# Optimization experiments

Hardware: AMD Instinct MI355X
Metric: run time of the kernel (lower is better)

Reference implementation:

```python
import jax, jax.numpy as jnp
import numpy as np

B, S, D, H = 2, 2048, 1024, 16
HD = D // H  # head dim = 64


def setup_inputs() -> dict:
    key = jax.random.key(0)
    ks = jax.random.split(key, 9)
    std = 0.02
    return {
        "hidden_states": jax.random.normal(ks[0], (B, S, D), jnp.float32),
        "wq": jax.random.normal(ks[1], (D, D), jnp.float32) * std,
        "bq": jnp.zeros((D,), jnp.float32),
        "wk": jax.random.normal(ks[2], (D, D), jnp.float32) * std,
        "bk": jnp.zeros((D,), jnp.float32),
        "wv": jax.random.normal(ks[3], (D, D), jnp.float32) * std,
        "bv": jnp.zeros((D,), jnp.float32),
        "wo": jax.random.normal(ks[4], (D, D), jnp.float32) * std,
        "bo": jnp.zeros((D,), jnp.float32),
    }


def reference(hidden_states, wq, bq, wk, bk, wv, bv, wo, bo):
    b, s, d = hidden_states.shape
    # projections (torch Linear: x @ W.T + b; here weights stored as [in,out]-equivalent transpose)
    q = hidden_states @ wq.T + bq
    k = hidden_states @ wk.T + bk
    v = hidden_states @ wv.T + bv
    # [b, h, s, hd]
    q = q.reshape(b, s, H, HD).transpose(0, 2, 1, 3)
    k = k.reshape(b, s, H, HD).transpose(0, 2, 1, 3)
    v = v.reshape(b, s, H, HD).transpose(0, 2, 1, 3)
    scores = jnp.einsum("bhqd,bhkd->bhqk", q, k) / jnp.sqrt(jnp.float32(HD))
    probs = jax.nn.softmax(scores, axis=-1)  # dropout p=0 (eval)
    ctx = jnp.einsum("bhqk,bhkd->bhqd", probs, v)
    ctx = ctx.transpose(0, 2, 1, 3).reshape(b, s, d)
    return ctx @ wo.T + bo
```

## Files before the change

### kernel.cpp

```cpp
#include <hip/hip_runtime.h>
#include <math.h>
#include <stdint.h>

constexpr int BB  = 2;
constexpr int SS  = 2048;
constexpr int DD  = 1024;
constexpr int HH  = 16;
constexpr int HDD = 64;
constexpr int MM  = BB * SS;

typedef uint16_t u16;
typedef __attribute__((ext_vector_type(4))) float    f32x4;
typedef __attribute__((ext_vector_type(8))) _Float16 f16x8;
typedef __attribute__((ext_vector_type(4))) _Float16 f16x4;
typedef __attribute__((ext_vector_type(8))) short    s16x8;
typedef __attribute__((ext_vector_type(4))) unsigned int u32x4;

__device__ __forceinline__ u16 to_f16(float f) {
    const _Float16 h = (_Float16)f;
    return __builtin_bit_cast(u16, h);
}

__device__ __forceinline__ f32x4 mfma32(s16x8 a, s16x8 b, f32x4 c) {
    return __builtin_amdgcn_mfma_f32_16x16x32_f16(
        __builtin_bit_cast(f16x8, a), __builtin_bit_cast(f16x8, b), c, 0, 0, 0);
}
__device__ __forceinline__ f32x4 mfma32_ff(s16x8 a, f16x8 b, f32x4 c) {
    return __builtin_amdgcn_mfma_f32_16x16x32_f16(
        __builtin_bit_cast(f16x8, a), b, c, 0, 0, 0);
}

__device__ __forceinline__ void load_lds16(const void* g, void* l) {
    __builtin_amdgcn_global_load_lds(
        (const __attribute__((address_space(1))) void*)g,
        (__attribute__((address_space(3))) void*)l, 16, 0, 0);
}

__global__ __launch_bounds__(256) void cast_all(
    const float* __restrict__ x,
    const float* __restrict__ w0, const float* __restrict__ w1,
    const float* __restrict__ w2, const float* __restrict__ w3,
    u16* __restrict__ xb, u16* __restrict__ wb)
{
    const int blk = blockIdx.x, tid = threadIdx.x;
    const float* src; u16* dst; int idx;
    if (blk < 2048) { src = x; dst = xb; idx = blk * 256 + tid; }
    else {
        const int b2 = blk - 2048, which = b2 >> 9;
        src = (which == 0) ? w0 : (which == 1) ? w1 : (which == 2) ? w2 : w3;
        dst = wb + ((size_t)which << 20);
        idx = (b2 & 511) * 256 + tid;
    }
    const float4* in4 = (const float4*)src;
    const float4 a = in4[idx * 2], b = in4[idx * 2 + 1];
    s16x8 v;
    v[0] = (short)to_f16(a.x); v[1] = (short)to_f16(a.y);
    v[2] = (short)to_f16(a.z); v[3] = (short)to_f16(a.w);
    v[4] = (short)to_f16(b.x); v[5] = (short)to_f16(b.y);
    v[6] = (short)to_f16(b.z); v[7] = (short)to_f16(b.w);
    *(s16x8*)(dst + (size_t)idx * 8) = v;
}

template <bool SWAP>
__device__ __forceinline__ void kloop(
    const u16* __restrict__ Ag, const u16* __restrict__ Wg,
    u16* Abase, u16* Bbase, const int K, const int KH,
    const int c0, const int c1,
    const int lane, const int wm, const int wn, f32x4 (&acc)[4][4])
{
    load_lds16(Ag + (size_t)c0 * 16 * K, Abase + c0 * 512);
    load_lds16(Ag + (size_t)c1 * 16 * K, Abase + c1 * 512);
    load_lds16(Wg + (size_t)c0 * 16 * K, Bbase + c0 * 512);
    load_lds16(Wg + (size_t)c1 * 16 * K, Bbase + c1 * 512);

    for (int k0 = 0; k0 < KH; k0 += 32) {
        const int buf = (k0 >> 5) & 1;
        __syncthreads();
        if (k0 + 32 < KH) {
            const int nb_ = (buf ^ 1) * 4096;
            load_lds16(Ag + (size_t)c0 * 16 * K + k0 + 32, Abase + nb_ + c0 * 512);
            load_lds16(Ag + (size_t)c1 * 16 * K + k0 + 32, Abase + nb_ + c1 * 512);
            load_lds16(Wg + (size_t)c0 * 16 * K + k0 + 32, Bbase + nb_ + c0 * 512);
            load_lds16(Wg + (size_t)c1 * 16 * K + k0 + 32, Bbase + nb_ + c1 * 512);
        }
        const u16* Acur = Abase + buf * 4096;
        const u16* Bcur = Bbase + buf * 4096;

        s16x8 af[4], bf4[4];
#pragma unroll
        for (int i = 0; i < 4; ++i) {
            const int row = wm + i * 16 + (lane & 15);
            const int u   = (lane >> 4) ^ (row & 3);
            af[i] = *(const s16x8*)(Acur + (size_t)row * 32 + u * 8);
        }
#pragma unroll
        for (int j = 0; j < 4; ++j) {
            const int row = wn + j * 16 + (lane & 15);
            const int u   = (lane >> 4) ^ (row & 3);
            bf4[j] = *(const s16x8*)(Bcur + (size_t)row * 32 + u * 8);
        }
#pragma unroll
        for (int i = 0; i < 4; ++i)
#pragma unroll
            for (int j = 0; j < 4; ++j)
                acc[i][j] = SWAP ? mfma32(bf4[j], af[i], acc[i][j])
                                 : mfma32(af[i], bf4[j], acc[i][j]);
    }
}

template <int MODE>
__global__ __launch_bounds__(512) void gemm_mfma(
    const u16* __restrict__ A, const u16* __restrict__ Wb,
    const float* __restrict__ b0, const float* __restrict__ b1,
    const float* __restrict__ b2,
    float* __restrict__ outf, u16* __restrict__ outq, u16* __restrict__ outv,
    const int K)
{
    __shared__ u16 smem[32768];
    u16* As = smem;
    u16* Bs = smem + 16384;

    const int tid = threadIdx.x, lane = tid & 63, wid = tid >> 6;
    const int grp = wid >> 2, w4 = wid & 3;
    const int quad = lane >> 4;
    const int bm = blockIdx.y * 128;
    const int nb = blockIdx.x * 128;
    const int which = nb >> 10;
    const int ncol  = nb & 1023;
    const int KH = K >> 1;
    const u16* Wblk = Wb + ((size_t)which << 20) + (size_t)ncol * K;

    const int srow = lane >> 2;
    const int lu   = (lane & 3) ^ (srow & 3);
    const u16* Ag = A    + (size_t)(bm + srow) * K + grp * KH + lu * 8;
    const u16* Wg = Wblk + (size_t)srow       * K + grp * KH + lu * 8;
    const int c0 = w4 * 2, c1 = c0 + 1;
    u16* Abase = As + grp * 8192;
    u16* Bbase = Bs + grp * 8192;

    f32x4 acc[4][4];
#pragma unroll
    for (int i = 0; i < 4; ++i)
#pragma unroll
        for (int j = 0; j < 4; ++j) { f32x4 z = {0.f, 0.f, 0.f, 0.f}; acc[i][j] = z; }

    const int wm = (w4 >> 1) * 64, wn = (w4 & 1) * 64;
    const bool swap = (MODE == 0) || (which < 2);
    if (swap) kloop<true>(Ag, Wg, Abase, Bbase, K, KH, c0, c1, lane, wm, wn, acc);
    else      kloop<false>(Ag, Wg, Abase, Bbase, K, KH, c0, c1, lane, wm, wn, acc);

    __syncthreads();
    float* rp = (float*)smem;
    const int slot = (w4 * 64 + lane) * 4;
    if (grp == 1) {
#pragma unroll
        for (int i = 0; i < 4; ++i)
#pragma unroll
            for (int j = 0; j < 4; ++j)
                *(f32x4*)(rp + (i * 4 + j) * 1024 + slot) = acc[i][j];
    }
    __syncthreads();
    if (grp != 0) return;
#pragma unroll
    for (int i = 0; i < 4; ++i)
#pragma unroll
        for (int j = 0; j < 4; ++j)
            acc[i][j] += *(const f32x4*)(rp + (i * 4 + j) * 1024 + slot);

    if (MODE == 0) {
#pragma unroll
        for (int j = 0; j < 4; ++j) {
            const int n0 = nb + wn + 16 * j + quad * 4;
            const float4 bv = *(const float4*)&b0[n0];
#pragma unroll
            for (int i = 0; i < 4; ++i) {
                const int m = bm + wm + 16 * i + (lane & 15);
                f32x4 w = acc[i][j];
                w[0] += bv.x; w[1] += bv.y; w[2] += bv.z; w[3] += bv.w;
                *(f32x4*)&outf[(size_t)m * 1024 + n0] = w;
            }
        }
    } else if (which < 2) {
        const float* bias = which ? b1 : b0;
        const float scale = which ? 1.0f : 0.125f;
        u16* outb = outq + ((size_t)which << 22);
        const int h = (ncol + wn) >> 6;
#pragma unroll
        for (int j = 0; j < 4; ++j) {
            const int nl0 = ncol + wn + 16 * j + quad * 4;
            const float4 bv = *(const float4*)&bias[nl0];
            const int hd0 = 16 * j + quad * 4;
#pragma unroll
            for (int i = 0; i < 4; ++i) {
                const int m = bm + wm + 16 * i + (lane & 15);
                const int b_ = m >> 11, s = m & 2047;
                f16x4 w;
                w[0] = (_Float16)((acc[i][j][0] + bv.x) * scale);
                w[1] = (_Float16)((acc[i][j][1] + bv.y) * scale);
                w[2] = (_Float16)((acc[i][j][2] + bv.z) * scale);
                w[3] = (_Float16)((acc[i][j][3] + bv.w) * scale);
                *(f16x4*)&outb[(((size_t)(b_ * HH + h)) * SS + s) * HDD + hd0] = w;
            }
        }
    } else {
        const int kt = ((bm + wm) & 2047) >> 6;
        const int b_ = (bm + wm) >> 11;
#pragma unroll
        for (int j = 0; j < 4; ++j) {
            const int nl = ncol + wn + 16 * j + (lane & 15);
            const float bb = b2[nl];
            const int h = nl >> 6, hd = nl & 63;
            u16* vrow = outv + (((size_t)(b_ * HH + h)) * HDD + hd) * SS + kt * 64;
#pragma unroll
            for (int i = 0; i < 4; ++i) {
                const int p0 = (i >> 1) * 32 + quad * 8 + (i & 1) * 4;
                f16x4 w;
                w[0] = (_Float16)(acc[i][j][0] + bb);
                w[1] = (_Float16)(acc[i][j][1] + bb);
                w[2] = (_Float16)(acc[i][j][2] + bb);
                w[3] = (_Float16)(acc[i][j][3] + bb);
                *(f16x4*)&vrow[p0] = w;
            }
        }
    }
}

__global__ __launch_bounds__(512, 4) void attn_mfma(
    const u16* __restrict__ Q, const u16* __restrict__ Kg,
    const u16* __restrict__ Vt, u16* __restrict__ ctx)
{
    __shared__ u16 smem[32768];

    const int tid = threadIdx.x, lane = tid & 63, wid = tid >> 6;
    const int grp = wid >> 2, w4 = wid & 3;
    const int quad = lane >> 4;
    const int bh = blockIdx.y, q0 = blockIdx.x * 128;
    const u16* Qb = Q  + (size_t)bh * SS * HDD;
    const u16* Kb = Kg + (size_t)bh * SS * HDD + (size_t)grp * 1024 * HDD;
    const u16* Vb = Vt + (size_t)bh * HDD * SS + grp * 1024;

    u16* Kbase = smem + grp * 8192;
    u16* Vbase = smem + 16384 + grp * 8192;

    const int qa = q0 + w4 * 32 + (lane & 15);
    const s16x8 bq0a = *(const s16x8*)(Qb + (size_t)qa * HDD + quad * 8);
    const s16x8 bq1a = *(const s16x8*)(Qb + (size_t)qa * HDD + 32 + quad * 8);
    const s16x8 bq0b = *(const s16x8*)(Qb + (size_t)(qa + 16) * HDD + quad * 8);
    const s16x8 bq1b = *(const s16x8*)(Qb + (size_t)(qa + 16) * HDD + 32 + quad * 8);

    f32x4 oa[4], ob[4];
    f32x4 la4 = {0.f, 0.f, 0.f, 0.f}, lb4 = {0.f, 0.f, 0.f, 0.f};
#pragma unroll
    for (int m = 0; m < 4; ++m) {
        f32x4 z = {0.f, 0.f, 0.f, 0.f};
        oa[m] = z; ob[m] = z;
    }
    const s16x8 ones = {15360, 15360, 15360, 15360,
                        15360, 15360, 15360, 15360};

    const int c0 = w4 * 2, c1 = c0 + 1;
    const int r0 = (c0 * 64 + lane) >> 3, lu0 = ((lane & 7) ^ (r0 & 7));
    const int r1 = (c1 * 64 + lane) >> 3, lu1 = ((lane & 7) ^ (r1 & 7));
    const u16* Kp0 = Kb + (size_t)r0 * HDD + lu0 * 8;
    const u16* Kp1 = Kb + (size_t)r1 * HDD + lu1 * 8;
    const u16* Vp0 = Vb + (size_t)r0 * SS + lu0 * 8;
    const u16* Vp1 = Vb + (size_t)r1 * SS + lu1 * 8;

    load_lds16(Kp0, Kbase + c0 * 512);
    load_lds16(Kp1, Kbase + c1 * 512);
    load_lds16(Vp0, Vbase + c0 * 512);
    load_lds16(Vp1, Vbase + c1 * 512);

    for (int kt = 0; kt < 16; ++kt) {
        const int buf = kt & 1;
        __syncthreads();

        if (kt + 1 < 16) {
            const int nb_ = (buf ^ 1) * 4096;
            load_lds16(Kp0 + (size_t)(kt + 1) * 64 * HDD, Kbase + nb_ + c0 * 512);
            load_lds16(Kp1 + (size_t)(kt + 1) * 64 * HDD, Kbase + nb_ + c1 * 512);
            load_lds16(Vp0 + (kt + 1) * 64, Vbase + nb_ + c0 * 512);
            load_lds16(Vp1 + (kt + 1) * 64, Vbase + nb_ + c1 * 512);
        }
        const u16* Kbuf = Kbase + buf * 4096;
        const u16* Vbuf = Vbase + buf * 4096;

        f32x4 Sa[4], Sb[4];
#pragma unroll
        for (int j = 0; j < 4; ++j) {
            const int row = j * 16 + (lane & 15);
            const int sw = lane & 7;
            const s16x8 ak0 = *(const s16x8*)(Kbuf + (size_t)row * 64 + ((quad    ) ^ sw) * 8);
            const s16x8 ak1 = *(const s16x8*)(Kbuf + (size_t)row * 64 + ((quad + 4) ^ sw) * 8);
            f32x4 za = {0.f, 0.f, 0.f, 0.f};
            za = mfma32(ak0, bq0a, za);
            za = mfma32(ak1, bq1a, za);
            Sa[j] = za;
            f32x4 zb = {0.f, 0.f, 0.f, 0.f};
            zb = mfma32(ak0, bq0b, zb);
            zb = mfma32(ak1, bq1b, zb);
            Sb[j] = zb;
        }

        f16x8 pb0a, pb1a, pb0b, pb1b;
        {
            u32x4 u;
            u[0] = __builtin_bit_cast(unsigned int, __builtin_amdgcn_cvt_pkrtz(__expf(Sa[0][0]), __expf(Sa[0][1])));
            u[1] = __builtin_bit_cast(unsigned int, __builtin_amdgcn_cvt_pkrtz(__expf(Sa[0][2]), __expf(Sa[0][3])));
            u[2] = __builtin_bit_cast(unsigned int, __builtin_amdgcn_cvt_pkrtz(__expf(Sa[1][0]), __expf(Sa[1][1])));
            u[3] = __builtin_bit_cast(unsigned int, __builtin_amdgcn_cvt_pkrtz(__expf(Sa[1][2]), __expf(Sa[1][3])));
            pb0a = __builtin_bit_cast(f16x8, u);
            u[0] = __builtin_bit_cast(unsigned int, __builtin_amdgcn_cvt_pkrtz(__expf(Sa[2][0]), __expf(Sa[2][1])));
            u[1] = __builtin_bit_cast(unsigned int, __builtin_amdgcn_cvt_pkrtz(__expf(Sa[2][2]), __expf(Sa[2][3])));
            u[2] = __builtin_bit_cast(unsigned int, __builtin_amdgcn_cvt_pkrtz(__expf(Sa[3][0]), __expf(Sa[3][1])));
            u[3] = __builtin_bit_cast(unsigned int, __builtin_amdgcn_cvt_pkrtz(__expf(Sa[3][2]), __expf(Sa[3][3])));
            pb1a = __builtin_bit_cast(f16x8, u);
            u[0] = __builtin_bit_cast(unsigned int, __builtin_amdgcn_cvt_pkrtz(__expf(Sb[0][0]), __expf(Sb[0][1])));
            u[1] = __builtin_bit_cast(unsigned int, __builtin_amdgcn_cvt_pkrtz(__expf(Sb[0][2]), __expf(Sb[0][3])));
            u[2] = __builtin_bit_cast(unsigned int, __builtin_amdgcn_cvt_pkrtz(__expf(Sb[1][0]), __expf(Sb[1][1])));
            u[3] = __builtin_bit_cast(unsigned int, __builtin_amdgcn_cvt_pkrtz(__expf(Sb[1][2]), __expf(Sb[1][3])));
            pb0b = __builtin_bit_cast(f16x8, u);
            u[0] = __builtin_bit_cast(unsigned int, __builtin_amdgcn_cvt_pkrtz(__expf(Sb[2][0]), __expf(Sb[2][1])));
            u[1] = __builtin_bit_cast(unsigned int, __builtin_amdgcn_cvt_pkrtz(__expf(Sb[2][2]), __expf(Sb[2][3])));
            u[2] = __builtin_bit_cast(unsigned int, __builtin_amdgcn_cvt_pkrtz(__expf(Sb[3][0]), __expf(Sb[3][1])));
            u[3] = __builtin_bit_cast(unsigned int, __builtin_amdgcn_cvt_pkrtz(__expf(Sb[3][2]), __expf(Sb[3][3])));
            pb1b = __builtin_bit_cast(f16x8, u);
        }

        la4 = mfma32_ff(ones, pb0a, la4);
        la4 = mfma32_ff(ones, pb1a, la4);
        lb4 = mfma32_ff(ones, pb0b, lb4);
        lb4 = mfma32_ff(ones, pb1b, lb4);

#pragma unroll
        for (int m = 0; m < 4; ++m) {
            const int row = m * 16 + (lane & 15);
            const int sw = lane & 7;
            const s16x8 v0 = *(const s16x8*)(Vbuf + (size_t)row * 64 + ((quad    ) ^ sw) * 8);
            const s16x8 v1 = *(const s16x8*)(Vbuf + (size_t)row * 64 + ((quad + 4) ^ sw) * 8);
            oa[m] = mfma32_ff(v0, pb0a, oa[m]);
            oa[m] = mfma32_ff(v1, pb1a, oa[m]);
            ob[m] = mfma32_ff(v0, pb0b, ob[m]);
            ob[m] = mfma32_ff(v1, pb1b, ob[m]);
        }
    }

    __syncthreads();
    float* ep = (float*)smem;
    float* lp = ep + 8 * 1088;
    if (grp == 1) {
#pragma unroll
        for (int sub = 0; sub < 2; ++sub) {
            const float* src = (sub == 0) ? (const float*)&oa[0] : (const float*)&ob[0];
            float* base = ep + (w4 * 2 + sub) * 1088 + (lane & 15) * 68 + quad * 4;
#pragma unroll
            for (int m = 0; m < 4; ++m)
                *(f32x4*)(base + m * 16) = *(const f32x4*)(src + m * 4);
        }
        if (quad == 0) {
            lp[(w4 * 2 + 0) * 16 + (lane & 15)] = la4[0];
            lp[(w4 * 2 + 1) * 16 + (lane & 15)] = lb4[0];
        }
    }
    __syncthreads();
    if (grp == 0) {
        const int b_ = bh >> 4, h = bh & 15;
#pragma unroll
        for (int sub = 0; sub < 2; ++sub) {
            const f32x4* own = (sub == 0) ? &oa[0] : &ob[0];
            const float lown = (sub == 0) ? la4[0] : lb4[0];
            const float inv = 1.f / (lown + lp[(w4 * 2 + sub) * 16 + (lane & 15)]);
            const float* base = ep + (w4 * 2 + sub) * 1088 + (lane & 15) * 68 + quad * 4;
            const int s_idx = q0 + w4 * 32 + sub * 16 + (lane & 15);
            u16* orow = ctx + ((size_t)(b_ * SS + s_idx)) * DD + h * HDD;
#pragma unroll
            for (int m = 0; m < 4; ++m) {
                const f32x4 part = *(const f32x4*)(base + m * 16);
                f16x4 w;
#pragma unroll
                for (int r = 0; r < 4; ++r)
                    w[r] = (_Float16)((own[m][r] + part[r]) * inv);
                *(f16x4*)(orow + m * 16 + quad * 4) = w;
            }
        }
    }
}

extern "C" void kernel_launch(void* const* d_in, const int* in_sizes, int n_in,
                              void* d_out, int out_size, void* d_ws, size_t ws_size,
                              hipStream_t stream)
{
    const float* x  = (const float*)d_in[0];
    const float* wq = (const float*)d_in[1];
    const float* bq = (const float*)d_in[2];
    const float* wk = (const float*)d_in[3];
    const float* bk = (const float*)d_in[4];
    const float* wv = (const float*)d_in[5];
    const float* bv = (const float*)d_in[6];
    const float* wo = (const float*)d_in[7];
    const float* bo = (const float*)d_in[8];

    u16* xb   = (u16*)d_ws;
    u16* wb   = xb  + ((size_t)4  << 20);
    u16* qk   = wb  + ((size_t)4  << 20);
    u16* vtw  = qk  + ((size_t)8  << 20);
    u16* ctxb = vtw + ((size_t)4  << 20);

    cast_all<<<4096, 256, 0, stream>>>(x, wq, wk, wv, wo, xb, wb);

    gemm_mfma<1><<<dim3(24, 32), 512, 0, stream>>>(
        xb, wb, bq, bk, bv, nullptr, qk, vtw, DD);

    attn_mfma<<<dim3(16, 32), 512, 0, stream>>>(
        qk, qk + ((size_t)4 << 20), vtw, ctxb);

    gemm_mfma<0><<<dim3(8, 32), 512, 0, stream>>>(
        ctxb, wb + ((size_t)3 << 20), bo, nullptr, nullptr,
        (float*)d_out, nullptr, nullptr, DD);
}
```

Baseline: 193.6 us.

## Replace QKV projection GEMM with 256x256-tile, 4-stage pipelined MFMA kernel

Adds a dedicated QKV projection kernel that uses 256x256 output tiles instead of 128x128 with a split-K reduction. It streams A and B through a 4-deep LDS ring filled by direct global-to-LDS loads, synchronised with explicit waitcnt and barriers, and raises wave priority around the MFMA bursts. Blocks are remapped so that consecutive workgroups share input tiles, aiming to improve cache reuse. The goal is to raise arithmetic intensity and hide global-load latency in the largest GEMM; the costs are 128 KB of LDS per block, heavy register use for the 8x4 accumulators, and fewer blocks (192) than before. The output GEMM is split into its own simplified kernel.

```diff
diff --git a/kernel.cpp b/kernel.cpp
--- a/kernel.cpp
+++ b/kernel.cpp
@@ -35,6 +35,14 @@
         (const __attribute__((address_space(1))) void*)g,
         (__attribute__((address_space(3))) void*)l, 16, 0, 0);
 }
+
+#define BARRIER() do { __builtin_amdgcn_sched_barrier(0); \
+                       __builtin_amdgcn_s_barrier();      \
+                       __builtin_amdgcn_sched_barrier(0); } while (0)
+#define LGKM0()   do { asm volatile("s_waitcnt lgkmcnt(0)" ::: "memory"); \
+                       __builtin_amdgcn_sched_barrier(0); } while (0)
+#define VMCNT(n)  do { asm volatile("s_waitcnt vmcnt(" #n ")" ::: "memory"); \
+                       __builtin_amdgcn_sched_barrier(0); } while (0)
 
 __global__ __launch_bounds__(256) void cast_all(
     const float* __restrict__ x,
@@ -59,6 +67,172 @@
     v[4] = (short)to_f16(b.x); v[5] = (short)to_f16(b.y);
     v[6] = (short)to_f16(b.z); v[7] = (short)to_f16(b.w);
     *(s16x8*)(dst + (size_t)idx * 8) = v;
+}
+
+template <bool SWAP>
+__device__ __forceinline__ void qkv_pipe(
+    const u16* __restrict__ pA0, const u16* __restrict__ pA1,
+    const u16* __restrict__ pB0, const u16* __restrict__ pB1,
+    u16* ldsA, u16* ldsB, const int stA,
+    const int (&aofs)[8], const int (&bofs)[4], f32x4 (&acc)[8][4])
+{
+#define STAGE_A(t_, s_) do { \
+    load_lds16(pA0 + (t_) * 32, ldsA + (s_) * 8192 + stA);        \
+    load_lds16(pA1 + (t_) * 32, ldsA + (s_) * 8192 + 4096 + stA); } while (0)
+#define STAGE_B(t_, s_) do { \
+    load_lds16(pB0 + (t_) * 32, ldsB + (s_) * 8192 + stA);        \
+    load_lds16(pB1 + (t_) * 32, ldsB + (s_) * 8192 + 4096 + stA); } while (0)
+
+    STAGE_A(0, 0); STAGE_B(0, 0);
+    STAGE_A(1, 1); STAGE_B(1, 1);
+    STAGE_A(2, 2); STAGE_B(2, 2);
+    VMCNT(8);
+    BARRIER();
+
+#pragma unroll 1
+    for (int t = 0; t < 32; ++t) {
+        const int so = (t & 3) * 8192;
+        const u16* A_ = ldsA + so;
+        const u16* B_ = ldsB + so;
+
+        s16x8 Af[4], Bf[4];
+#pragma unroll
+        for (int m = 0; m < 4; ++m) Af[m] = *(const s16x8*)(A_ + aofs[m]);
+#pragma unroll
+        for (int n = 0; n < 4; ++n) Bf[n] = *(const s16x8*)(B_ + bofs[n]);
+        if (t + 3 < 32) STAGE_A(t + 3, (t + 3) & 3);
+        BARRIER(); LGKM0();
+        __builtin_amdgcn_s_setprio(1);
+#pragma unroll
+        for (int m = 0; m < 4; ++m)
+#pragma unroll
+            for (int n = 0; n < 4; ++n)
+                acc[m][n] = SWAP ? mfma32(Bf[n], Af[m], acc[m][n])
+                                 : mfma32(Af[m], Bf[n], acc[m][n]);
+        __builtin_amdgcn_s_setprio(0);
+        BARRIER();
+
+#pragma unroll
+        for (int m = 0; m < 4; ++m) Af[m] = *(const s16x8*)(A_ + aofs[m + 4]);
+        if (t + 3 < 32) STAGE_B(t + 3, (t + 3) & 3);
+        BARRIER(); LGKM0();
+        __builtin_amdgcn_s_setprio(1);
+#pragma unroll
+        for (int m = 0; m < 4; ++m)
+#pragma unroll
+            for (int n = 0; n < 4; ++n)
+                acc[m + 4][n] = SWAP ? mfma32(Bf[n], Af[m], acc[m + 4][n])
+                                     : mfma32(Af[m], Bf[n], acc[m + 4][n]);
+        __builtin_amdgcn_s_setprio(0);
+
+        if (t < 31) {
+            if (t < 29)       { VMCNT(8); }
+            else if (t == 29) { VMCNT(4); }
+            else              { VMCNT(0); }
+            BARRIER();
+        }
+    }
+#undef STAGE_A
+#undef STAGE_B
+}
+
+__global__ __launch_bounds__(512, 2) void qkv8(
+    const u16* __restrict__ A, const u16* __restrict__ Wb,
+    const float* __restrict__ bq_, const float* __restrict__ bk_,
+    const float* __restrict__ bv_,
+    u16* __restrict__ outq, u16* __restrict__ outv)
+{
+    __shared__ u16 smem[65536];
+    u16* ldsA = smem;
+    u16* ldsB = smem + 32768;
+
+    const int tid = threadIdx.x, lane = tid & 63, wid = tid >> 6;
+    const int lt = lane & 15, quad = lane >> 4;
+
+    const int orig = blockIdx.y * 12 + blockIdx.x;
+    const int wg   = (orig & 7) * 24 + (orig >> 3);
+    const int bxt  = wg % 12, byt = wg / 12;
+    const int bm = byt * 256, nb = bxt * 256;
+    const int which = nb >> 10;
+    const int ncol  = nb & 1023;
+    const u16* Wblk = Wb + ((size_t)which << 20) + (size_t)ncol * 1024;
+
+    const int pl = wid * 64 + lane;
+    const int r0 = pl >> 2;
+    const int gu = (lane & 3) ^ ((r0 ^ (r0 >> 2)) & 3);
+    const u16* pA0 = A    + (size_t)(bm + r0)       * 1024 + gu * 8;
+    const u16* pA1 = A    + (size_t)(bm + 128 + r0) * 1024 + gu * 8;
+    const u16* pB0 = Wblk + (size_t)r0              * 1024 + gu * 8;
+    const u16* pB1 = Wblk + (size_t)(128 + r0)      * 1024 + gu * 8;
+    const int stA = wid * 512;
+
+    const int WM = (wid >> 2) * 128, WN = (wid & 3) * 64;
+
+    int aofs[8], bofs[4];
+#pragma unroll
+    for (int m = 0; m < 8; ++m) {
+        const int row = WM + m * 16 + lt;
+        aofs[m] = row * 32 + ((quad ^ ((row ^ (row >> 2)) & 3)) * 8);
+    }
+#pragma unroll
+    for (int n = 0; n < 4; ++n) {
+        const int row = WN + n * 16 + lt;
+        bofs[n] = row * 32 + ((quad ^ ((row ^ (row >> 2)) & 3)) * 8);
+    }
+
+    f32x4 acc[8][4];
+#pragma unroll
+    for (int m = 0; m < 8; ++m)
+#pragma unroll
+        for (int n = 0; n < 4; ++n) { f32x4 z = {0.f, 0.f, 0.f, 0.f}; acc[m][n] = z; }
+
+    if (which < 2) qkv_pipe<true >(pA0, pA1, pB0, pB1, ldsA, ldsB, stA, aofs, bofs, acc);
+    else           qkv_pipe<false>(pA0, pA1, pB0, pB1, ldsA, ldsB, stA, aofs, bofs, acc);
+
+    if (which < 2) {
+        const float* bias = which ? bk_ : bq_;
+        const float scale = which ? 1.0f : 0.125f;
+        u16* outb = outq + ((size_t)which << 22);
+        const int h = (ncol + WN) >> 6;
+#pragma unroll
+        for (int j = 0; j < 4; ++j) {
+            const int nl0 = ncol + WN + 16 * j + quad * 4;
+            const float4 bv = *(const float4*)&bias[nl0];
+            const int hd0 = 16 * j + quad * 4;
+#pragma unroll
+            for (int m = 0; m < 8; ++m) {
+                const int mr = bm + WM + 16 * m + lt;
+                const int b_ = mr >> 11, s = mr & 2047;
+                f16x4 w;
+                w[0] = (_Float16)((acc[m][j][0] + bv.x) * scale);
+                w[1] = (_Float16)((acc[m][j][1] + bv.y) * scale);
+                w[2] = (_Float16)((acc[m][j][2] + bv.z) * scale);
+                w[3] = (_Float16)((acc[m][j][3] + bv.w) * scale);
+                *(f16x4*)&outb[(((size_t)(b_ * HH + h)) * SS + s) * HDD + hd0] = w;
+            }
+        }
+    } else {
+        const int b_  = (bm + WM) >> 11;
+        const int kt0 = ((bm + WM) & 2047) >> 6;
+#pragma unroll
+        for (int j = 0; j < 4; ++j) {
+            const int nl = ncol + WN + 16 * j + lt;
+            const float bb = bv_[nl];
+            const int h = nl >> 6, hd = nl & 63;
+            u16* vbase = outv + (((size_t)(b_ * HH + h)) * HDD + hd) * SS;
+#pragma unroll
+            for (int m = 0; m < 8; ++m) {
+                const int ii = m & 3;
+                const int p0 = (ii >> 1) * 32 + quad * 8 + (ii & 1) * 4;
+                f16x4 w;
+                w[0] = (_Float16)(acc[m][j][0] + bb);
+                w[1] = (_Float16)(acc[m][j][1] + bb);
+                w[2] = (_Float16)(acc[m][j][2] + bb);
+                w[3] = (_Float16)(acc[m][j][3] + bb);
+                *(f16x4*)&vbase[(kt0 + (m >> 2)) * 64 + p0] = w;
+            }
+        }
+    }
 }
 
 template <bool SWAP>
@@ -108,13 +282,9 @@
     }
 }
 
-template <int MODE>
-__global__ __launch_bounds__(512) void gemm_mfma(
+__global__ __launch_bounds__(512) void gemm_out(
     const u16* __restrict__ A, const u16* __restrict__ Wb,
-    const float* __restrict__ b0, const float* __restrict__ b1,
-    const float* __restrict__ b2,
-    float* __restrict__ outf, u16* __restrict__ outq, u16* __restrict__ outv,
-    const int K)
+    const float* __restrict__ b0, float* __restrict__ outf)
 {
     __shared__ u16 smem[32768];
     u16* As = smem;
@@ -125,10 +295,8 @@
     const int quad = lane >> 4;
     const int bm = blockIdx.y * 128;
     const int nb = blockIdx.x * 128;
-    const int which = nb >> 10;
-    const int ncol  = nb & 1023;
-    const int KH = K >> 1;
-    const u16* Wblk = Wb + ((size_t)which << 20) + (size_t)ncol * K;
+    const int K = 1024, KH = 512;
+    const u16* Wblk = Wb + (size_t)nb * K;
 
     const int srow = lane >> 2;
     const int lu   = (lane & 3) ^ (srow & 3);
@@ -145,9 +313,7 @@
         for (int j = 0; j < 4; ++j) { f32x4 z = {0.f, 0.f, 0.f, 0.f}; acc[i][j] = z; }
 
     const int wm = (w4 >> 1) * 64, wn = (w4 & 1) * 64;
-    const bool swap = (MODE == 0) || (which < 2);
-    if (swap) kloop<true>(Ag, Wg, Abase, Bbase, K, KH, c0, c1, lane, wm, wn, acc);
-    else      kloop<false>(Ag, Wg, Abase, Bbase, K, KH, c0, c1, lane, wm, wn, acc);
+    kloop<true>(Ag, Wg, Abase, Bbase, K, KH, c0, c1, lane, wm, wn, acc);
 
     __syncthreads();
     float* rp = (float*)smem;
@@ -167,60 +333,16 @@
         for (int j = 0; j < 4; ++j)
             acc[i][j] += *(const f32x4*)(rp + (i * 4 + j) * 1024 + slot);
 
-    if (MODE == 0) {
-#pragma unroll
-        for (int j = 0; j < 4; ++j) {
-            const int n0 = nb + wn + 16 * j + quad * 4;
-            const float4 bv = *(const float4*)&b0[n0];
-#pragma unroll
-            for (int i = 0; i < 4; ++i) {
-                const int m = bm + wm + 16 * i + (lane & 15);
-                f32x4 w = acc[i][j];
-                w[0] += bv.x; w[1] += bv.y; w[2] += bv.z; w[3] += bv.w;
-                *(f32x4*)&outf[(size_t)m * 1024 + n0] = w;
-            }
-        }
-    } else if (which < 2) {
-        const float* bias = which ? b1 : b0;
-        const float scale = which ? 1.0f : 0.125f;
-        u16* outb = outq + ((size_t)which << 22);
-        const int h = (ncol + wn) >> 6;
-#pragma unroll
-        for (int j = 0; j < 4; ++j) {
-            const int nl0 = ncol + wn + 16 * j + quad * 4;
-            const float4 bv = *(const float4*)&bias[nl0];
-            const int hd0 = 16 * j + quad * 4;
-#pragma unroll
-            for (int i = 0; i < 4; ++i) {
-                const int m = bm + wm + 16 * i + (lane & 15);
-                const int b_ = m >> 11, s = m & 2047;
-                f16x4 w;
-                w[0] = (_Float16)((acc[i][j][0] + bv.x) * scale);
-                w[1] = (_Float16)((acc[i][j][1] + bv.y) * scale);
-                w[2] = (_Float16)((acc[i][j][2] + bv.z) * scale);
-                w[3] = (_Float16)((acc[i][j][3] + bv.w) * scale);
-                *(f16x4*)&outb[(((size_t)(b_ * HH + h)) * SS + s) * HDD + hd0] = w;
-            }
-        }
-    } else {
-        const int kt = ((bm + wm) & 2047) >> 6;
-        const int b_ = (bm + wm) >> 11;
-#pragma unroll
-        for (int j = 0; j < 4; ++j) {
-            const int nl = ncol + wn + 16 * j + (lane & 15);
-            const float bb = b2[nl];
-            const int h = nl >> 6, hd = nl & 63;
-            u16* vrow = outv + (((size_t)(b_ * HH + h)) * HDD + hd) * SS + kt * 64;
-#pragma unroll
-            for (int i = 0; i < 4; ++i) {
-                const int p0 = (i >> 1) * 32 + quad * 8 + (i & 1) * 4;
-                f16x4 w;
-                w[0] = (_Float16)(acc[i][j][0] + bb);
-                w[1] = (_Float16)(acc[i][j][1] + bb);
-                w[2] = (_Float16)(acc[i][j][2] + bb);
-                w[3] = (_Float16)(acc[i][j][3] + bb);
-                *(f16x4*)&vrow[p0] = w;
-            }
+#pragma unroll
+    for (int j = 0; j < 4; ++j) {
+        const int n0 = nb + wn + 16 * j + quad * 4;
+        const float4 bv = *(const float4*)&b0[n0];
+#pragma unroll
+        for (int i = 0; i < 4; ++i) {
+            const int m = bm + wm + 16 * i + (lane & 15);
+            f32x4 w = acc[i][j];
+            w[0] += bv.x; w[1] += bv.y; w[2] += bv.z; w[3] += bv.w;
+            *(f32x4*)&outf[(size_t)m * 1024 + n0] = w;
         }
     }
 }
@@ -408,13 +530,11 @@
 
     cast_all<<<4096, 256, 0, stream>>>(x, wq, wk, wv, wo, xb, wb);
 
-    gemm_mfma<1><<<dim3(24, 32), 512, 0, stream>>>(
-        xb, wb, bq, bk, bv, nullptr, qk, vtw, DD);
+    qkv8<<<dim3(12, 16), 512, 0, stream>>>(xb, wb, bq, bk, bv, qk, vtw);
 
     attn_mfma<<<dim3(16, 32), 512, 0, stream>>>(
         qk, qk + ((size_t)4 << 20), vtw, ctxb);
 
-    gemm_mfma<0><<<dim3(8, 32), 512, 0, stream>>>(
-        ctxb, wb + ((size_t)3 << 20), bo, nullptr, nullptr,
-        (float*)d_out, nullptr, nullptr, DD);
-}
+    gemm_out<<<dim3(8, 32), 512, 0, stream>>>(
+        ctxb, wb + ((size_t)3 << 20), bo, (float*)d_out);
+}
```

Result: no change. 196.5 us (+1.5%).

## Deepen GEMM K-tile to 64 with 8-way swizzle and XCD-aware block remap

Applied to the files above, without the earlier changes.

The projection GEMM k-loop now stages 64-wide K slices per buffer instead of 32, which halves the number of barrier iterations and issues two MFMAs per accumulator per stage. The LDS layout moves to an 8-way XOR swizzle over 64-element rows, and shared memory grows to 128 KB. Block indices are remapped so that consecutive workgroups land on the same XCD slice of the tile grid, which is meant to improve L2 reuse. The larger LDS footprint may limit occupancy to one block per CU, and K is now hardcoded to 1024.

```diff
diff --git a/kernel.cpp b/kernel.cpp
--- a/kernel.cpp
+++ b/kernel.cpp
@@ -62,50 +62,63 @@
 }
 
 template <bool SWAP>
-__device__ __forceinline__ void kloop(
+__device__ __forceinline__ void kloop64(
     const u16* __restrict__ Ag, const u16* __restrict__ Wg,
-    u16* Abase, u16* Bbase, const int K, const int KH,
-    const int c0, const int c1,
+    u16* Abase, u16* Bbase, const int w4,
     const int lane, const int wm, const int wn, f32x4 (&acc)[4][4])
 {
-    load_lds16(Ag + (size_t)c0 * 16 * K, Abase + c0 * 512);
-    load_lds16(Ag + (size_t)c1 * 16 * K, Abase + c1 * 512);
-    load_lds16(Wg + (size_t)c0 * 16 * K, Bbase + c0 * 512);
-    load_lds16(Wg + (size_t)c1 * 16 * K, Bbase + c1 * 512);
-
-    for (int k0 = 0; k0 < KH; k0 += 32) {
-        const int buf = (k0 >> 5) & 1;
+    const int lt = lane & 15, quad = lane >> 4;
+    const int cb = w4 * 4;
+
+#define STG64(buf_, ko_) do {                                              \
+    _Pragma("unroll")                                                      \
+    for (int c = 0; c < 4; ++c) {                                          \
+        load_lds16(Ag + (size_t)((cb + c) * 8) * 1024 + (ko_),             \
+                   Abase + (buf_) * 8192 + (cb + c) * 512);                \
+        load_lds16(Wg + (size_t)((cb + c) * 8) * 1024 + (ko_),             \
+                   Bbase + (buf_) * 8192 + (cb + c) * 512);                \
+    } } while (0)
+
+    STG64(0, 0);
+
+#pragma unroll 1
+    for (int it = 0; it < 8; ++it) {
+        const int buf = it & 1;
         __syncthreads();
-        if (k0 + 32 < KH) {
-            const int nb_ = (buf ^ 1) * 4096;
-            load_lds16(Ag + (size_t)c0 * 16 * K + k0 + 32, Abase + nb_ + c0 * 512);
-            load_lds16(Ag + (size_t)c1 * 16 * K + k0 + 32, Abase + nb_ + c1 * 512);
-            load_lds16(Wg + (size_t)c0 * 16 * K + k0 + 32, Bbase + nb_ + c0 * 512);
-            load_lds16(Wg + (size_t)c1 * 16 * K + k0 + 32, Bbase + nb_ + c1 * 512);
-        }
-        const u16* Acur = Abase + buf * 4096;
-        const u16* Bcur = Bbase + buf * 4096;
-
-        s16x8 af[4], bf4[4];
-#pragma unroll
-        for (int i = 0; i < 4; ++i) {
-            const int row = wm + i * 16 + (lane & 15);
-            const int u   = (lane >> 4) ^ (row & 3);
-            af[i] = *(const s16x8*)(Acur + (size_t)row * 32 + u * 8);
-        }
-#pragma unroll
-        for (int j = 0; j < 4; ++j) {
-            const int row = wn + j * 16 + (lane & 15);
-            const int u   = (lane >> 4) ^ (row & 3);
-            bf4[j] = *(const s16x8*)(Bcur + (size_t)row * 32 + u * 8);
+        if (it < 7) STG64(buf ^ 1, (it + 1) * 64);
+        const u16* Acur = Abase + buf * 8192;
+        const u16* Bcur = Bbase + buf * 8192;
+
+        s16x8 af[2][4], bf[2][4];
+#pragma unroll
+        for (int kk = 0; kk < 2; ++kk) {
+#pragma unroll
+            for (int i = 0; i < 4; ++i) {
+                const int row = wm + i * 16 + lt;
+                af[kk][i] = *(const s16x8*)(Acur + row * 64 +
+                                (((kk * 4 + quad) ^ (row & 7)) * 8));
+            }
+#pragma unroll
+            for (int j = 0; j < 4; ++j) {
+                const int row = wn + j * 16 + lt;
+                bf[kk][j] = *(const s16x8*)(Bcur + row * 64 +
+                                (((kk * 4 + quad) ^ (row & 7)) * 8));
+            }
         }
 #pragma unroll
         for (int i = 0; i < 4; ++i)
 #pragma unroll
-            for (int j = 0; j < 4; ++j)
-                acc[i][j] = SWAP ? mfma32(bf4[j], af[i], acc[i][j])
-                                 : mfma32(af[i], bf4[j], acc[i][j]);
-    }
+            for (int j = 0; j < 4; ++j) {
+                if (SWAP) {
+                    acc[i][j] = mfma32(bf[0][j], af[0][i], acc[i][j]);
+                    acc[i][j] = mfma32(bf[1][j], af[1][i], acc[i][j]);
+                } else {
+                    acc[i][j] = mfma32(af[0][i], bf[0][j], acc[i][j]);
+                    acc[i][j] = mfma32(af[1][i], bf[1][j], acc[i][j]);
+                }
+            }
+    }
+#undef STG64
 }
 
 template <int MODE>
@@ -113,30 +126,31 @@
     const u16* __restrict__ A, const u16* __restrict__ Wb,
     const float* __restrict__ b0, const float* __restrict__ b1,
     const float* __restrict__ b2,
-    float* __restrict__ outf, u16* __restrict__ outq, u16* __restrict__ outv,
-    const int K)
+    float* __restrict__ outf, u16* __restrict__ outq, u16* __restrict__ outv)
 {
-    __shared__ u16 smem[32768];
-    u16* As = smem;
-    u16* Bs = smem + 16384;
+    __shared__ u16 smem[65536];
 
     const int tid = threadIdx.x, lane = tid & 63, wid = tid >> 6;
     const int grp = wid >> 2, w4 = wid & 3;
     const int quad = lane >> 4;
-    const int bm = blockIdx.y * 128;
-    const int nb = blockIdx.x * 128;
+
+    constexpr int NBX = (MODE == 1) ? 24 : 8;
+    constexpr int CPX = (MODE == 1) ? 96 : 32;
+    const int orig = blockIdx.y * NBX + blockIdx.x;
+    const int wg   = (orig & 7) * CPX + (orig >> 3);
+    const int bxt  = wg % NBX, byt = wg / NBX;
+    const int bm = byt * 128;
+    const int nb = bxt * 128;
     const int which = nb >> 10;
     const int ncol  = nb & 1023;
-    const int KH = K >> 1;
-    const u16* Wblk = Wb + ((size_t)which << 20) + (size_t)ncol * K;
-
-    const int srow = lane >> 2;
-    const int lu   = (lane & 3) ^ (srow & 3);
-    const u16* Ag = A    + (size_t)(bm + srow) * K + grp * KH + lu * 8;
-    const u16* Wg = Wblk + (size_t)srow       * K + grp * KH + lu * 8;
-    const int c0 = w4 * 2, c1 = c0 + 1;
-    u16* Abase = As + grp * 8192;
-    u16* Bbase = Bs + grp * 8192;
+    const u16* Wblk = Wb + ((size_t)which << 20) + (size_t)ncol * 1024;
+
+    const int rbase = lane >> 3;
+    const int gu    = (lane & 7) ^ rbase;
+    const u16* Ag = A    + (size_t)(bm + rbase) * 1024 + grp * 512 + gu * 8;
+    const u16* Wg = Wblk + (size_t)rbase        * 1024 + grp * 512 + gu * 8;
+    u16* Abase = smem + grp * 16384;
+    u16* Bbase = smem + 32768 + grp * 16384;
 
     f32x4 acc[4][4];
 #pragma unroll
@@ -146,8 +160,8 @@
 
     const int wm = (w4 >> 1) * 64, wn = (w4 & 1) * 64;
     const bool swap = (MODE == 0) || (which < 2);
-    if (swap) kloop<true>(Ag, Wg, Abase, Bbase, K, KH, c0, c1, lane, wm, wn, acc);
-    else      kloop<false>(Ag, Wg, Abase, Bbase, K, KH, c0, c1, lane, wm, wn, acc);
+    if (swap) kloop64<true >(Ag, Wg, Abase, Bbase, w4, lane, wm, wn, acc);
+    else      kloop64<false>(Ag, Wg, Abase, Bbase, w4, lane, wm, wn, acc);
 
     __syncthreads();
     float* rp = (float*)smem;
@@ -409,12 +423,12 @@
     cast_all<<<4096, 256, 0, stream>>>(x, wq, wk, wv, wo, xb, wb);
 
     gemm_mfma<1><<<dim3(24, 32), 512, 0, stream>>>(
-        xb, wb, bq, bk, bv, nullptr, qk, vtw, DD);
+        xb, wb, bq, bk, bv, nullptr, qk, vtw);
 
     attn_mfma<<<dim3(16, 32), 512, 0, stream>>>(
         qk, qk + ((size_t)4 << 20), vtw, ctxb);
 
     gemm_mfma<0><<<dim3(8, 32), 512, 0, stream>>>(
         ctxb, wb + ((size_t)3 << 20), bo, nullptr, nullptr,
-        (float*)d_out, nullptr, nullptr, DD);
-}
+        (float*)d_out, nullptr, nullptr);
+}
```

After: 187.6 us. -3.1%, faster.
